# Kernel tuning notes

Hardware: AMD Instinct MI355X
Metric: run time of the kernel (lower is better)

## Reference

```python
import jax, jax.numpy as jnp
import numpy as np

T, IN, H = 16384, 1024, 4096   # tokens, in_features, hidden_features
G = 64                          # quantization group size (nunchaku default)
R = 32                          # LoRA rank for SVDQuant low-rank branch


def _dequant_weight(qw, ws):
    # qw: [out, in] int4 values in [-8,7] (stored int32); ws: [out, in//G] per-group scales
    out, inn = qw.shape
    w = qw.astype(jnp.float32).reshape(out, inn // G, G) * ws[:, :, None]
    return w.reshape(out, inn)


def _qdq_act(x):
    # simulate per-token, per-group int4 quantize->dequantize of activations
    t, d = x.shape
    xg = x.reshape(t, d // G, G)
    s = jnp.maximum(jnp.max(jnp.abs(xg), axis=-1, keepdims=True), 1e-6) / 7.0
    q = jnp.clip(jnp.round(xg / s), -8.0, 7.0)
    return (q * s).reshape(t, d)


def _svdquant_linear(x, qw, ws, smooth, ld, lu, b):
    # quantized main branch on smoothed input + full-precision LoRA correction on raw input
    xq = _qdq_act(x / smooth)                      # [T, d_in]
    w = _dequant_weight(qw, ws)                    # [d_out, d_in]
    main = jnp.einsum('td,od->to', xq, w)          # int4-sim GEMM
    lora = jnp.einsum('tr,or->to', jnp.einsum('td,rd->tr', x, ld), lu)
    return main + lora + b


def setup_inputs() -> dict:
    key = jax.random.key(0)
    ks = jax.random.split(key, 12)
    x = jax.random.normal(ks[0], (T, IN), dtype=jnp.float32)
    qw1 = jax.random.randint(ks[1], (H, IN), -8, 8, dtype=jnp.int32)
    ws1 = jax.random.uniform(ks[2], (H, IN // G), dtype=jnp.float32) * 0.01 + 0.001
    smooth1 = jax.random.uniform(ks[3], (IN,), dtype=jnp.float32) + 0.5
    ld1 = jax.random.normal(ks[4], (R, IN), dtype=jnp.float32) * 0.02
    lu1 = jax.random.normal(ks[5], (H, R), dtype=jnp.float32) * 0.02
    b1 = jax.random.normal(ks[6], (H,), dtype=jnp.float32) * 0.01
    qw2 = jax.random.randint(ks[7], (IN, H), -8, 8, dtype=jnp.int32)
    ws2 = jax.random.uniform(ks[8], (IN, H // G), dtype=jnp.float32) * 0.01 + 0.001
    smooth2 = jax.random.uniform(ks[9], (H,), dtype=jnp.float32) + 0.5
    ld2 = jax.random.normal(ks[10], (R, H), dtype=jnp.float32) * 0.02
    lu2 = jax.random.normal(ks[11], (IN, R), dtype=jnp.float32) * 0.02
    b2 = jnp.zeros((IN,), dtype=jnp.float32)
    return {"x": x, "qw1": qw1, "ws1": ws1, "smooth1": smooth1, "ld1": ld1,
            "lu1": lu1, "b1": b1, "qw2": qw2, "ws2": ws2, "smooth2": smooth2,
            "ld2": ld2, "lu2": lu2, "b2": b2}


def reference(x, qw1, ws1, smooth1, ld1, lu1, b1, qw2, ws2, smooth2, ld2, lu2, b2):
    h = _svdquant_linear(x, qw1, ws1, smooth1, ld1, lu1, b1)   # fc1
    h = jax.nn.gelu(h, approximate=True)                        # fused GELU
    y = _svdquant_linear(h, qw2, ws2, smooth2, ld2, lu2, b2)   # fc2
    return y
```

## Files before the change

### kernel.cpp

```cpp
#include <hip/hip_runtime.h>
#include <math.h>

#define T_TOK 16384
#define D_IN  1024
#define D_H   4096
#define GQ    64
#define R_L   32
#define NPANEL 4
#define PANW   (D_H / NPANEL)

typedef __attribute__((ext_vector_type(8))) __bf16 bf16x8;
typedef __attribute__((ext_vector_type(4))) float  f32x4;
typedef __attribute__((ext_vector_type(8))) unsigned short ushort8;

__device__ __forceinline__ unsigned short f2bf(float f) {
  union { float f; unsigned u; } v; v.f = f;
  unsigned u = v.u + 0x7FFFu + ((v.u >> 16) & 1u);
  return (unsigned short)(u >> 16);
}

__device__ __forceinline__ float bf2f(unsigned short h) {
  union { unsigned u; float f; } v; v.u = ((unsigned)h) << 16; return v.f;
}

__device__ __forceinline__ void gload_lds16(const unsigned short* g, unsigned short* l) {
  __builtin_amdgcn_global_load_lds(
      (const __attribute__((address_space(1))) unsigned int*)g,
      (__attribute__((address_space(3))) unsigned int*)l, 16, 0, 0);
}

__device__ __forceinline__ float gelu_tanh(float v) {
  float u = 0.7978845608028654f * (v + 0.044715f * v * v * v);
  return 0.5f * v * (1.0f + tanhf(u));
}

__global__ __launch_bounds__(256)
void convert_kernel(const int* __restrict__ qw1, const int* __restrict__ qw2,
                    unsigned short* __restrict__ qw1b, unsigned short* __restrict__ qw2b) {
  const size_t N1 = (size_t)D_H * D_IN;
  const size_t N2 = (size_t)D_IN * D_H;
  const size_t total = N1 + N2;
  for (size_t i = (size_t)blockIdx.x * 256 + threadIdx.x; i < total;
       i += (size_t)gridDim.x * 256) {
    if (i < N1) qw1b[i]    = f2bf((float)qw1[i]);
    else        qw2b[i-N1] = f2bf((float)qw2[i-N1]);
  }
}

__global__ __launch_bounds__(256)
void prep1_kernel(const float* __restrict__ x, const float* __restrict__ smooth,
                  const float* __restrict__ ld,
                  unsigned short* __restrict__ qx, float* __restrict__ sx,
                  float* __restrict__ xrf) {
  __shared__ float xrow[D_IN];
  const int t = blockIdx.x;
  const int tid = threadIdx.x;
  float4 x4  = *(const float4*)(x + (size_t)t * D_IN + tid * 4);
  float4 sm4 = *(const float4*)(smooth + tid * 4);
  *(float4*)&xrow[tid * 4] = x4;
  double z0 = (double)x4.x / (double)sm4.x;
  double z1 = (double)x4.y / (double)sm4.y;
  double z2 = (double)x4.z / (double)sm4.z;
  double z3 = (double)x4.w / (double)sm4.w;
  double amax = fmax(fmax(fabs(z0), fabs(z1)), fmax(fabs(z2), fabs(z3)));
#pragma unroll
  for (int d = 1; d < 16; d <<= 1) amax = fmax(amax, __shfl_xor(amax, d, 16));
  double s = fmax(amax, 1e-6) / 7.0;
  double q0 = fmin(fmax(rint(z0 / s), -8.0), 7.0);
  double q1 = fmin(fmax(rint(z1 / s), -8.0), 7.0);
  double q2 = fmin(fmax(rint(z2 / s), -8.0), 7.0);
  double q3 = fmin(fmax(rint(z3 / s), -8.0), 7.0);
  ushort4 qu; qu.x = f2bf((float)q0); qu.y = f2bf((float)q1);
  qu.z = f2bf((float)q2); qu.w = f2bf((float)q3);
  *(ushort4*)(qx + (size_t)t * D_IN + tid * 4) = qu;
  if ((tid & 15) == 0) sx[(size_t)t * (D_IN / GQ) + (tid >> 4)] = (float)s;
  __syncthreads();
  const int w = tid >> 6, l = tid & 63;
#pragma unroll
  for (int rr = 0; rr < 8; ++rr) {
    int r = w * 8 + rr;
    const float* ldr = ld + (size_t)r * D_IN;
    double sum = 0.0;
#pragma unroll
    for (int k = 0; k < 16; ++k)
      sum = fma((double)xrow[l + 64 * k], (double)ldr[l + 64 * k], sum);
#pragma unroll
    for (int d = 32; d >= 1; d >>= 1) sum += __shfl_xor(sum, d, 64);
    if (l == 0) xrf[(size_t)t * R_L + r] = (float)sum;
  }
}

__global__ __launch_bounds__(512, 2)
void gemm_fc1(const unsigned short* __restrict__ Aq,
              const float* __restrict__ Asx,
              const unsigned short* __restrict__ Bq,
              const float* __restrict__ Bws,
              const float* __restrict__ xrf,
              const float* __restrict__ lu1,
              const float* __restrict__ b1,
              const float* __restrict__ smooth2,
              int c0base,
              unsigned short* __restrict__ hb,
              unsigned short* __restrict__ qx2,
              float* __restrict__ sx2) {
  __shared__ unsigned short As[2][128 * 64];
  __shared__ unsigned short Bs[2][128 * 64];
  __shared__ float sxd[2][128];
  __shared__ float wss[2][128];
  const int tid = threadIdx.x;
  const int lane = tid & 63;
  const int wid = tid >> 6;
  const int wr = wid >> 1;
  const int wc = wid & 1;
  const int l15 = lane & 15, l4 = lane >> 4;
  const int lin = blockIdx.y * 8 + blockIdx.x;
  const int sw  = (lin & 7) * 128 + (lin >> 3);
  const int t0 = (sw >> 3) * 128;
  const int c0 = c0base + (sw & 7) * 128;

  float acc[2][4][4] = {};
  const int srow = tid >> 3;
  const int schk = tid & 7;
  const int ske  = schk * 8;
  const int sswz = (schk ^ (srow & 7)) * 8;

#pragma unroll
  for (int q = 0; q < 2; ++q) {
    int row = q * 64 + srow;
    gload_lds16(Aq + (long)(t0 + row) * D_IN + sswz, &As[0][row * 64 + ske]);
    gload_lds16(Bq + (long)(c0 + row) * D_IN + sswz, &Bs[0][row * 64 + ske]);
  }
  if (tid < 128)      sxd[0][tid] = Asx[(long)(t0 + tid) * 16 + 0];
  else if (tid < 256) wss[0][tid - 128] = Bws[(long)(c0 + tid - 128) * 16 + 0];

  int cur = 0;
  for (int g = 0; g < 16; ++g) {
    __syncthreads();

    if (g < 15) {
      const int kn = (g + 1) * 64;
      const int nb = cur ^ 1;
#pragma unroll
      for (int q = 0; q < 2; ++q) {
        int row = q * 64 + srow;
        gload_lds16(Aq + (long)(t0 + row) * D_IN + kn + sswz,
                    &As[nb][row * 64 + ske]);
        gload_lds16(Bq + (long)(c0 + row) * D_IN + kn + sswz,
                    &Bs[nb][row * 64 + ske]);
      }
      if (tid < 128)      sxd[nb][tid] = Asx[(long)(t0 + tid) * 16 + (g + 1)];
      else if (tid < 256) wss[nb][tid - 128] = Bws[(long)(c0 + tid - 128) * 16 + (g + 1)];
    }

    float sd[2][4];
#pragma unroll
    for (int m = 0; m < 2; ++m)
#pragma unroll
      for (int jj = 0; jj < 4; ++jj)
        sd[m][jj] = sxd[cur][wr * 32 + m * 16 + l4 * 4 + jj];
    float wd[4];
#pragma unroll
    for (int n = 0; n < 4; ++n)
      wd[n] = wss[cur][wc * 64 + n * 16 + l15];

    bf16x8 af[2][2], bfr[4][2];
#pragma unroll
    for (int m = 0; m < 2; ++m) {
      const int r = wr * 32 + m * 16 + l15;
      const unsigned short* base = &As[cur][r * 64];
      af[m][0] = *(const bf16x8*)(base + ((l4    ) ^ (r & 7)) * 8);
      af[m][1] = *(const bf16x8*)(base + ((l4 + 4) ^ (r & 7)) * 8);
    }
#pragma unroll
    for (int n = 0; n < 4; ++n) {
      const int r = wc * 64 + n * 16 + l15;
      const unsigned short* base = &Bs[cur][r * 64];
      bfr[n][0] = *(const bf16x8*)(base + ((l4    ) ^ (r & 7)) * 8);
      bfr[n][1] = *(const bf16x8*)(base + ((l4 + 4) ^ (r & 7)) * 8);
    }

#pragma unroll
    for (int m = 0; m < 2; ++m) {
#pragma unroll
      for (int n = 0; n < 4; ++n) {
        f32x4 t = {0.f, 0.f, 0.f, 0.f};
        t = __builtin_amdgcn_mfma_f32_16x16x32_bf16(af[m][0], bfr[n][0], t, 0, 0, 0);
        t = __builtin_amdgcn_mfma_f32_16x16x32_bf16(af[m][1], bfr[n][1], t, 0, 0, 0);
#pragma unroll
        for (int j = 0; j < 4; ++j)
          acc[m][n][j] = fmaf(t[j], sd[m][j] * wd[n], acc[m][n][j]);
      }
    }
    cur ^= 1;
  }

  __syncthreads();
  float* xr_lds = (float*)&As[0][0];
  float* lu_lds = (float*)&Bs[0][0];
  {
    const int row = tid >> 2;
    const int q4  = (tid & 3) * 8;
    const float4 a0 = *(const float4*)(xrf + (size_t)(t0 + row) * R_L + q4);
    const float4 a1 = *(const float4*)(xrf + (size_t)(t0 + row) * R_L + q4 + 4);
    *(float4*)&xr_lds[row * 36 + q4]     = a0;
    *(float4*)&xr_lds[row * 36 + q4 + 4] = a1;
    const float4 b0 = *(const float4*)(lu1 + (size_t)(c0 + row) * R_L + q4);
    const float4 b1v = *(const float4*)(lu1 + (size_t)(c0 + row) * R_L + q4 + 4);
    *(float4*)&lu_lds[row * 36 + q4]     = b0;
    *(float4*)&lu_lds[row * 36 + q4 + 4] = b1v;
  }
  __syncthreads();

  float bv[4], rsmv[4];
  int colL[4];
#pragma unroll
  for (int n = 0; n < 4; ++n) {
    int col = c0 + wc * 64 + n * 16 + l15;
    colL[n] = wc * 64 + n * 16 + l15;
    bv[n] = b1[col];
    rsmv[n] = 1.0f / smooth2[col];
  }
  const int clocal0 = c0 - c0base;

#pragma unroll
  for (int m = 0; m < 2; ++m) {
#pragma unroll
    for (int j = 0; j < 4; ++j) {
      const int rloc = wr * 32 + m * 16 + l4 * 4 + j;
      const int trow = t0 + rloc;
      float lor[4] = {0.f, 0.f, 0.f, 0.f};
#pragma unroll
      for (int k = 0; k < 8; ++k) {
        const float4 xq = *(const float4*)&xr_lds[rloc * 36 + k * 4];
#pragma unroll
        for (int n = 0; n < 4; ++n) {
          const float4 lc = *(const float4*)&lu_lds[colL[n] * 36 + k * 4];
          lor[n] = fmaf(xq.x, lc.x, lor[n]);
          lor[n] = fmaf(xq.y, lc.y, lor[n]);
          lor[n] = fmaf(xq.z, lc.z, lor[n]);
          lor[n] = fmaf(xq.w, lc.w, lor[n]);
        }
      }
      float hv[4], z[4];
      float amax = 0.f;
#pragma unroll
      for (int n = 0; n < 4; ++n) {
        float v = acc[m][n][j] + lor[n] + bv[n];
        v = gelu_tanh(v);
        hv[n] = v;
        z[n] = v * rsmv[n];
        amax = fmaxf(amax, fabsf(z[n]));
      }
#pragma unroll
      for (int d = 1; d < 16; d <<= 1) amax = fmaxf(amax, __shfl_xor(amax, d, 16));
      float s = fmaxf(amax, 1e-6f) / 7.0f;
      float rs = 1.0f / s;
#pragma unroll
      for (int n = 0; n < 4; ++n) {
        int coll = clocal0 + wc * 64 + n * 16 + l15;
        hb[(size_t)trow * PANW + coll] = f2bf(hv[n]);
        float qv = fminf(fmaxf(rintf(z[n] * rs), -8.f), 7.f);
        qx2[(size_t)trow * PANW + coll] = f2bf(qv);
      }
      if (l15 == 0)
        sx2[(size_t)trow * (PANW / GQ) + ((clocal0 + wc * 64) >> 6)] = s;
    }
  }
}

__global__ __launch_bounds__(256, 2)
void gemm_fc2(const unsigned short* __restrict__ Aq,
              const float* __restrict__ Asx,
              const unsigned short* __restrict__ Bq,
              int kB0,
              const float* __restrict__ Bws,
              int gB0,
              float* __restrict__ Yout, int first) {
  __shared__ unsigned short As[128 * 64];
  __shared__ unsigned short Bs[128 * 64];
  __shared__ float sxs[128];
  __shared__ float wss[128];
  const int tid = threadIdx.x;
  const int lane = tid & 63;
  const int wid = tid >> 6;
  const int wr = wid >> 1, wc = wid & 1;
  const int l15 = lane & 15, l4 = lane >> 4;
  const int lin = blockIdx.y * 8 + blockIdx.x;
  const int sw  = (lin & 7) * 128 + (lin >> 3);
  const int t0 = (sw >> 3) * 128;
  const int c0 = (sw & 7) * 128;

  f32x4 acc[4][4] = {};
  const int srow = tid >> 3;
  const int ske = (tid & 7) * 8;

  for (int g = 0; g < 16; ++g) {
    const int kA = g * 64 + ske;
    const int kB = kB0 + kA;
#pragma unroll
    for (int i = 0; i < 4; ++i) {
      int row = i * 32 + srow;
      gload_lds16(Aq + (long)(t0 + row) * PANW + kA, As + row * 64 + ske);
      gload_lds16(Bq + (long)(c0 + row) * D_H + kB, Bs + row * 64 + ske);
    }
    if (tid < 128) sxs[tid] = Asx[(long)(t0 + tid) * (PANW / GQ) + g];
    else           wss[tid - 128] = Bws[(long)(c0 + tid - 128) * (D_H / GQ) + gB0 + g];
    __syncthreads();

    bf16x8 af[4][2], bfr[4][2];
#pragma unroll
    for (int m = 0; m < 4; ++m) {
      const unsigned short* base = As + (wr * 64 + m * 16 + l15) * 64 + l4 * 8;
      af[m][0] = *(const bf16x8*)(base);
      af[m][1] = *(const bf16x8*)(base + 32);
    }
#pragma unroll
    for (int n = 0; n < 4; ++n) {
      const unsigned short* base = Bs + (wc * 64 + n * 16 + l15) * 64 + l4 * 8;
      bfr[n][0] = *(const bf16x8*)(base);
      bfr[n][1] = *(const bf16x8*)(base + 32);
    }
    f32x4 rsv[4];
#pragma unroll
    for (int m = 0; m < 4; ++m) rsv[m] = *(const f32x4*)&sxs[wr * 64 + m * 16 + l4 * 4];
    float csv[4];
#pragma unroll
    for (int n = 0; n < 4; ++n) csv[n] = wss[wc * 64 + n * 16 + l15];

#pragma unroll
    for (int m = 0; m < 4; ++m) {
#pragma unroll
      for (int n = 0; n < 4; ++n) {
        f32x4 t = {0.f, 0.f, 0.f, 0.f};
        t = __builtin_amdgcn_mfma_f32_16x16x32_bf16(af[m][0], bfr[n][0], t, 0, 0, 0);
        t = __builtin_amdgcn_mfma_f32_16x16x32_bf16(af[m][1], bfr[n][1], t, 0, 0, 0);
#pragma unroll
        for (int j = 0; j < 4; ++j)
          acc[m][n][j] += t[j] * (rsv[m][j] * csv[n]);
      }
    }
    __syncthreads();
  }

#pragma unroll
  for (int m = 0; m < 4; ++m)
#pragma unroll
    for (int n = 0; n < 4; ++n) {
      int col = c0 + wc * 64 + n * 16 + l15;
#pragma unroll
      for (int j = 0; j < 4; ++j) {
        int trow = t0 + wr * 64 + m * 16 + l4 * 4 + j;
        size_t idx = (size_t)trow * D_IN + col;
        float v = acc[m][n][j];
        if (!first) v += Yout[idx];
        Yout[idx] = v;
      }
    }
}

__global__ __launch_bounds__(256)
void xr2_simple(const unsigned short* __restrict__ hp,
                const float* __restrict__ ld2,
                int c0base,
                float* __restrict__ xracc,
                int first) {
  __shared__ unsigned short hs[8][PANW + 8];
  const int tid = threadIdx.x;
  const int t0 = blockIdx.x * 8;
#pragma unroll
  for (int q = 0; q < 4; ++q) {
    int v = tid + 256 * q;
    int row = v >> 7;
    int col = (v & 127) * 8;
    *(ushort8*)(&hs[row][col]) =
        *(const ushort8*)(hp + (size_t)(t0 + row) * PANW + col);
  }
  __syncthreads();
  const int tloc = tid & 7;
  const int r    = tid >> 3;
  const float* ldr = ld2 + (size_t)r * D_H + c0base;
  float sum = 0.f;
  for (int k8 = 0; k8 < PANW / 8; ++k8) {
    ushort8 hv = *(const ushort8*)(&hs[tloc][k8 * 8]);
    float4 w0 = *(const float4*)(ldr + k8 * 8);
    float4 w1 = *(const float4*)(ldr + k8 * 8 + 4);
    sum = fmaf(bf2f(hv[0]), w0.x, sum);
    sum = fmaf(bf2f(hv[1]), w0.y, sum);
    sum = fmaf(bf2f(hv[2]), w0.z, sum);
    sum = fmaf(bf2f(hv[3]), w0.w, sum);
    sum = fmaf(bf2f(hv[4]), w1.x, sum);
    sum = fmaf(bf2f(hv[5]), w1.y, sum);
    sum = fmaf(bf2f(hv[6]), w1.z, sum);
    sum = fmaf(bf2f(hv[7]), w1.w, sum);
  }
  size_t idx = (size_t)(t0 + tloc) * R_L + r;
  xracc[idx] = (first ? 0.f : xracc[idx]) + sum;
}

__global__ __launch_bounds__(256)
void finish_kernel(const float* __restrict__ xracc,
                   const float* __restrict__ lu2,
                   const float* __restrict__ b2,
                   float* __restrict__ Yout) {
  __shared__ float xls[16][R_L];
  const int tid = threadIdx.x;
  const int o   = blockIdx.x * 256 + tid;
  const int t0r = blockIdx.y * 16;
  for (int q = tid; q < 16 * R_L; q += 256)
    xls[q >> 5][q & 31] = xracc[(size_t)(t0r + (q >> 5)) * R_L + (q & 31)];
  float lr[R_L];
#pragma unroll
  for (int r = 0; r < R_L; ++r) lr[r] = lu2[(size_t)o * R_L + r];
  const float b2v = b2[o];
  __syncthreads();
#pragma unroll
  for (int i = 0; i < 16; ++i) {
    size_t idx = (size_t)(t0r + i) * D_IN + o;
    float v = Yout[idx] + b2v;
#pragma unroll
    for (int r = 0; r < R_L; ++r) v = fmaf(lr[r], xls[i][r], v);
    Yout[idx] = v;
  }
}

extern "C" void kernel_launch(void* const* d_in, const int* in_sizes, int n_in,
                              void* d_out, int out_size, void* d_ws, size_t ws_size,
                              hipStream_t stream) {
  const float* x       = (const float*)d_in[0];
  const int*   qw1     = (const int*)d_in[1];
  const float* ws1     = (const float*)d_in[2];
  const float* smooth1 = (const float*)d_in[3];
  const float* ld1     = (const float*)d_in[4];
  const float* lu1     = (const float*)d_in[5];
  const float* b1      = (const float*)d_in[6];
  const int*   qw2     = (const int*)d_in[7];
  const float* ws2     = (const float*)d_in[8];
  const float* smooth2 = (const float*)d_in[9];
  const float* ld2     = (const float*)d_in[10];
  const float* lu2     = (const float*)d_in[11];
  const float* b2      = (const float*)d_in[12];

  char* w = (char*)d_ws;
  size_t off = 0;
  auto take = [&](size_t bytes) {
    char* p = w + off;
    off = (off + bytes + 255) & ~(size_t)255;
    return p;
  };

  unsigned short* qw1b = (unsigned short*)take((size_t)D_H * D_IN * 2);
  unsigned short* qw2b = (unsigned short*)take((size_t)D_IN * D_H * 2);
  unsigned short* qx1  = (unsigned short*)take((size_t)T_TOK * D_IN * 2);
  float*          sx1  = (float*)take((size_t)T_TOK * (D_IN / GQ) * 4);
  float*          xr1f = (float*)take((size_t)T_TOK * R_L * 4);
  unsigned short* hp   = (unsigned short*)take((size_t)T_TOK * PANW * 2);
  unsigned short* qx2p = (unsigned short*)take((size_t)T_TOK * PANW * 2);
  float*          sx2  = (float*)take((size_t)T_TOK * (PANW / GQ) * 4);
  float*          xr2a = (float*)take((size_t)T_TOK * R_L * 4);
  (void)ws_size; (void)in_sizes; (void)n_in; (void)out_size;

  convert_kernel<<<2048, 256, 0, stream>>>(qw1, qw2, qw1b, qw2b);
  prep1_kernel<<<T_TOK, 256, 0, stream>>>(x, smooth1, ld1, qx1, sx1, xr1f);

  for (int p = 0; p < NPANEL; ++p) {
    const int c0base = p * PANW;
    const int first = (p == 0);

    dim3 g1(PANW / 128, T_TOK / 128);
    gemm_fc1<<<g1, 512, 0, stream>>>(qx1, sx1, qw1b, ws1, xr1f, lu1, b1, smooth2,
                                     c0base, hp, qx2p, sx2);

    xr2_simple<<<T_TOK / 8, 256, 0, stream>>>(hp, ld2, c0base, xr2a, first);

    dim3 g2(D_IN / 128, T_TOK / 128);
    gemm_fc2<<<g2, 256, 0, stream>>>(qx2p, sx2, qw2b, c0base, ws2, p * (PANW / GQ),
                                     (float*)d_out, first);
  }

  dim3 gf(D_IN / 256, T_TOK / 16);
  finish_kernel<<<gf, 256, 0, stream>>>(xr2a, lu2, b2, (float*)d_out);
}
```

Before: 1.297 ms.

## Double-buffer fc2 GEMM with swizzled LDS, fuse LoRA/bias epilogue, float prep dot

```diff
diff --git a/kernel.cpp b/kernel.cpp
--- a/kernel.cpp
+++ b/kernel.cpp
@@ -80,13 +80,13 @@
   for (int rr = 0; rr < 8; ++rr) {
     int r = w * 8 + rr;
     const float* ldr = ld + (size_t)r * D_IN;
-    double sum = 0.0;
+    float sum = 0.f;
 #pragma unroll
     for (int k = 0; k < 16; ++k)
-      sum = fma((double)xrow[l + 64 * k], (double)ldr[l + 64 * k], sum);
+      sum = fmaf(xrow[l + 64 * k], ldr[l + 64 * k], sum);
 #pragma unroll
     for (int d = 32; d >= 1; d >>= 1) sum += __shfl_xor(sum, d, 64);
-    if (l == 0) xrf[(size_t)t * R_L + r] = (float)sum;
+    if (l == 0) xrf[(size_t)t * R_L + r] = sum;
   }
 }
 
@@ -268,67 +268,95 @@
   }
 }
 
-__global__ __launch_bounds__(256, 2)
+__global__ __launch_bounds__(512, 2)
 void gemm_fc2(const unsigned short* __restrict__ Aq,
               const float* __restrict__ Asx,
               const unsigned short* __restrict__ Bq,
               int kB0,
               const float* __restrict__ Bws,
               int gB0,
-              float* __restrict__ Yout, int first) {
-  __shared__ unsigned short As[128 * 64];
-  __shared__ unsigned short Bs[128 * 64];
-  __shared__ float sxs[128];
-  __shared__ float wss[128];
+              const float* __restrict__ xr2a,
+              const float* __restrict__ lu2,
+              const float* __restrict__ b2,
+              float* __restrict__ Yout, int first, int last) {
+  __shared__ unsigned short As[2][128 * 64];
+  __shared__ unsigned short Bs[2][128 * 64];
+  __shared__ float sxd[2][128];
+  __shared__ float wss[2][128];
   const int tid = threadIdx.x;
   const int lane = tid & 63;
   const int wid = tid >> 6;
-  const int wr = wid >> 1, wc = wid & 1;
+  const int wr = wid >> 1;
+  const int wc = wid & 1;
   const int l15 = lane & 15, l4 = lane >> 4;
   const int lin = blockIdx.y * 8 + blockIdx.x;
   const int sw  = (lin & 7) * 128 + (lin >> 3);
   const int t0 = (sw >> 3) * 128;
   const int c0 = (sw & 7) * 128;
 
-  f32x4 acc[4][4] = {};
+  float acc[2][4][4] = {};
   const int srow = tid >> 3;
-  const int ske = (tid & 7) * 8;
-
+  const int schk = tid & 7;
+  const int ske  = schk * 8;
+  const int sswz = (schk ^ (srow & 7)) * 8;
+
+#pragma unroll
+  for (int q = 0; q < 2; ++q) {
+    int row = q * 64 + srow;
+    gload_lds16(Aq + (long)(t0 + row) * PANW + sswz, &As[0][row * 64 + ske]);
+    gload_lds16(Bq + (long)(c0 + row) * D_H + kB0 + sswz, &Bs[0][row * 64 + ske]);
+  }
+  if (tid < 128)      sxd[0][tid] = Asx[(long)(t0 + tid) * (PANW / GQ) + 0];
+  else if (tid < 256) wss[0][tid - 128] = Bws[(long)(c0 + tid - 128) * (D_H / GQ) + gB0 + 0];
+
+  int cur = 0;
   for (int g = 0; g < 16; ++g) {
-    const int kA = g * 64 + ske;
-    const int kB = kB0 + kA;
-#pragma unroll
-    for (int i = 0; i < 4; ++i) {
-      int row = i * 32 + srow;
-      gload_lds16(Aq + (long)(t0 + row) * PANW + kA, As + row * 64 + ske);
-      gload_lds16(Bq + (long)(c0 + row) * D_H + kB, Bs + row * 64 + ske);
-    }
-    if (tid < 128) sxs[tid] = Asx[(long)(t0 + tid) * (PANW / GQ) + g];
-    else           wss[tid - 128] = Bws[(long)(c0 + tid - 128) * (D_H / GQ) + gB0 + g];
     __syncthreads();
 
-    bf16x8 af[4][2], bfr[4][2];
-#pragma unroll
-    for (int m = 0; m < 4; ++m) {
-      const unsigned short* base = As + (wr * 64 + m * 16 + l15) * 64 + l4 * 8;
-      af[m][0] = *(const bf16x8*)(base);
-      af[m][1] = *(const bf16x8*)(base + 32);
+    if (g < 15) {
+      const int kn = (g + 1) * 64;
+      const int nb = cur ^ 1;
+#pragma unroll
+      for (int q = 0; q < 2; ++q) {
+        int row = q * 64 + srow;
+        gload_lds16(Aq + (long)(t0 + row) * PANW + kn + sswz,
+                    &As[nb][row * 64 + ske]);
+        gload_lds16(Bq + (long)(c0 + row) * D_H + kB0 + kn + sswz,
+                    &Bs[nb][row * 64 + ske]);
+      }
+      if (tid < 128)      sxd[nb][tid] = Asx[(long)(t0 + tid) * (PANW / GQ) + (g + 1)];
+      else if (tid < 256) wss[nb][tid - 128] = Bws[(long)(c0 + tid - 128) * (D_H / GQ) + gB0 + (g + 1)];
+    }
+
+    float sd[2][4];
+#pragma unroll
+    for (int m = 0; m < 2; ++m)
+#pragma unroll
+      for (int jj = 0; jj < 4; ++jj)
+        sd[m][jj] = sxd[cur][wr * 32 + m * 16 + l4 * 4 + jj];
+    float wd[4];
+#pragma unroll
+    for (int n = 0; n < 4; ++n)
+      wd[n] = wss[cur][wc * 64 + n * 16 + l15];
+
+    bf16x8 af[2][2], bfr[4][2];
+#pragma unroll
+    for (int m = 0; m < 2; ++m) {
+      const int r = wr * 32 + m * 16 + l15;
+      const unsigned short* base = &As[cur][r * 64];
+      af[m][0] = *(const bf16x8*)(base + ((l4    ) ^ (r & 7)) * 8);
+      af[m][1] = *(const bf16x8*)(base + ((l4 + 4) ^ (r & 7)) * 8);
     }
 #pragma unroll
     for (int n = 0; n < 4; ++n) {
-      const unsigned short* base = Bs + (wc * 64 + n * 16 + l15) * 64 + l4 * 8;
-      bfr[n][0] = *(const bf16x8*)(base);
-      bfr[n][1] = *(const bf16x8*)(base + 32);
-    }
-    f32x4 rsv[4];
-#pragma unroll
-    for (int m = 0; m < 4; ++m) rsv[m] = *(const f32x4*)&sxs[wr * 64 + m * 16 + l4 * 4];
-    float csv[4];
-#pragma unroll
-    for (int n = 0; n < 4; ++n) csv[n] = wss[wc * 64 + n * 16 + l15];
-
-#pragma unroll
-    for (int m = 0; m < 4; ++m) {
+      const int r = wc * 64 + n * 16 + l15;
+      const unsigned short* base = &Bs[cur][r * 64];
+      bfr[n][0] = *(const bf16x8*)(base + ((l4    ) ^ (r & 7)) * 8);
+      bfr[n][1] = *(const bf16x8*)(base + ((l4 + 4) ^ (r & 7)) * 8);
+    }
+
+#pragma unroll
+    for (int m = 0; m < 2; ++m) {
 #pragma unroll
       for (int n = 0; n < 4; ++n) {
         f32x4 t = {0.f, 0.f, 0.f, 0.f};
@@ -336,26 +364,79 @@
         t = __builtin_amdgcn_mfma_f32_16x16x32_bf16(af[m][1], bfr[n][1], t, 0, 0, 0);
 #pragma unroll
         for (int j = 0; j < 4; ++j)
-          acc[m][n][j] += t[j] * (rsv[m][j] * csv[n]);
-      }
-    }
+          acc[m][n][j] = fmaf(t[j], sd[m][j] * wd[n], acc[m][n][j]);
+      }
+    }
+    cur ^= 1;
+  }
+
+  if (last) {
     __syncthreads();
-  }
-
-#pragma unroll
-  for (int m = 0; m < 4; ++m)
+    float* xr_lds = (float*)&As[0][0];
+    float* lu_lds = (float*)&Bs[0][0];
+    {
+      const int row = tid >> 2;
+      const int q4  = (tid & 3) * 8;
+      const float4 a0 = *(const float4*)(xr2a + (size_t)(t0 + row) * R_L + q4);
+      const float4 a1 = *(const float4*)(xr2a + (size_t)(t0 + row) * R_L + q4 + 4);
+      *(float4*)&xr_lds[row * 36 + q4]     = a0;
+      *(float4*)&xr_lds[row * 36 + q4 + 4] = a1;
+      const float4 b0 = *(const float4*)(lu2 + (size_t)(c0 + row) * R_L + q4);
+      const float4 b1v = *(const float4*)(lu2 + (size_t)(c0 + row) * R_L + q4 + 4);
+      *(float4*)&lu_lds[row * 36 + q4]     = b0;
+      *(float4*)&lu_lds[row * 36 + q4 + 4] = b1v;
+    }
+    __syncthreads();
+
+    float bv[4];
+    int colL[4];
 #pragma unroll
     for (int n = 0; n < 4; ++n) {
-      int col = c0 + wc * 64 + n * 16 + l15;
+      colL[n] = wc * 64 + n * 16 + l15;
+      bv[n] = b2[c0 + colL[n]];
+    }
+#pragma unroll
+    for (int m = 0; m < 2; ++m) {
 #pragma unroll
       for (int j = 0; j < 4; ++j) {
-        int trow = t0 + wr * 64 + m * 16 + l4 * 4 + j;
-        size_t idx = (size_t)trow * D_IN + col;
-        float v = acc[m][n][j];
-        if (!first) v += Yout[idx];
-        Yout[idx] = v;
-      }
-    }
+        const int rloc = wr * 32 + m * 16 + l4 * 4 + j;
+        const int trow = t0 + rloc;
+        float lor[4] = {0.f, 0.f, 0.f, 0.f};
+#pragma unroll
+        for (int k = 0; k < 8; ++k) {
+          const float4 xq = *(const float4*)&xr_lds[rloc * 36 + k * 4];
+#pragma unroll
+          for (int n = 0; n < 4; ++n) {
+            const float4 lc = *(const float4*)&lu_lds[colL[n] * 36 + k * 4];
+            lor[n] = fmaf(xq.x, lc.x, lor[n]);
+            lor[n] = fmaf(xq.y, lc.y, lor[n]);
+            lor[n] = fmaf(xq.z, lc.z, lor[n]);
+            lor[n] = fmaf(xq.w, lc.w, lor[n]);
+          }
+        }
+#pragma unroll
+        for (int n = 0; n < 4; ++n) {
+          size_t idx = (size_t)trow * D_IN + c0 + colL[n];
+          Yout[idx] = Yout[idx] + acc[m][n][j] + lor[n] + bv[n];
+        }
+      }
+    }
+  } else {
+#pragma unroll
+    for (int m = 0; m < 2; ++m)
+#pragma unroll
+      for (int n = 0; n < 4; ++n) {
+        int col = c0 + wc * 64 + n * 16 + l15;
+#pragma unroll
+        for (int j = 0; j < 4; ++j) {
+          int trow = t0 + wr * 32 + m * 16 + l4 * 4 + j;
+          size_t idx = (size_t)trow * D_IN + col;
+          float v = acc[m][n][j];
+          if (!first) v += Yout[idx];
+          Yout[idx] = v;
+        }
+      }
+  }
 }
 
 __global__ __launch_bounds__(256)
@@ -397,32 +478,6 @@
   xracc[idx] = (first ? 0.f : xracc[idx]) + sum;
 }
 
-__global__ __launch_bounds__(256)
-void finish_kernel(const float* __restrict__ xracc,
-                   const float* __restrict__ lu2,
-                   const float* __restrict__ b2,
-                   float* __restrict__ Yout) {
-  __shared__ float xls[16][R_L];
-  const int tid = threadIdx.x;
-  const int o   = blockIdx.x * 256 + tid;
-  const int t0r = blockIdx.y * 16;
-  for (int q = tid; q < 16 * R_L; q += 256)
-    xls[q >> 5][q & 31] = xracc[(size_t)(t0r + (q >> 5)) * R_L + (q & 31)];
-  float lr[R_L];
-#pragma unroll
-  for (int r = 0; r < R_L; ++r) lr[r] = lu2[(size_t)o * R_L + r];
-  const float b2v = b2[o];
-  __syncthreads();
-#pragma unroll
-  for (int i = 0; i < 16; ++i) {
-    size_t idx = (size_t)(t0r + i) * D_IN + o;
-    float v = Yout[idx] + b2v;
-#pragma unroll
-    for (int r = 0; r < R_L; ++r) v = fmaf(lr[r], xls[i][r], v);
-    Yout[idx] = v;
-  }
-}
-
 extern "C" void kernel_launch(void* const* d_in, const int* in_sizes, int n_in,
                               void* d_out, int out_size, void* d_ws, size_t ws_size,
                               hipStream_t stream) {
@@ -464,7 +519,7 @@
 
   for (int p = 0; p < NPANEL; ++p) {
     const int c0base = p * PANW;
-    const int first = (p == 0);
+    const int first = (p == 0), last = (p == NPANEL - 1);
 
     dim3 g1(PANW / 128, T_TOK / 128);
     gemm_fc1<<<g1, 512, 0, stream>>>(qx1, sx1, qw1b, ws1, xr1f, lu1, b1, smooth2,
@@ -473,10 +528,7 @@
     xr2_simple<<<T_TOK / 8, 256, 0, stream>>>(hp, ld2, c0base, xr2a, first);
 
     dim3 g2(D_IN / 128, T_TOK / 128);
-    gemm_fc2<<<g2, 256, 0, stream>>>(qx2p, sx2, qw2b, c0base, ws2, p * (PANW / GQ),
-                                     (float*)d_out, first);
-  }
-
-  dim3 gf(D_IN / 256, T_TOK / 16);
-  finish_kernel<<<gf, 256, 0, stream>>>(xr2a, lu2, b2, (float*)d_out);
-}
+    gemm_fc2<<<g2, 512, 0, stream>>>(qx2p, sx2, qw2b, c0base, ws2, p * (PANW / GQ),
+                                     xr2a, lu2, b2, (float*)d_out, first, last);
+  }
+}
```

Measured after the change: 1.380 ms (median of 2 runs). +6.4%, slower.

## Rework fc1 GEMM to 256 threads, single-buffered LDS, larger per-warp tiles

Applied to the files above, without the earlier changes.

```diff
diff --git a/kernel.cpp b/kernel.cpp
--- a/kernel.cpp
+++ b/kernel.cpp
@@ -80,17 +80,17 @@
   for (int rr = 0; rr < 8; ++rr) {
     int r = w * 8 + rr;
     const float* ldr = ld + (size_t)r * D_IN;
-    double sum = 0.0;
+    float sum = 0.f;
 #pragma unroll
     for (int k = 0; k < 16; ++k)
-      sum = fma((double)xrow[l + 64 * k], (double)ldr[l + 64 * k], sum);
+      sum = fmaf(xrow[l + 64 * k], ldr[l + 64 * k], sum);
 #pragma unroll
     for (int d = 32; d >= 1; d >>= 1) sum += __shfl_xor(sum, d, 64);
-    if (l == 0) xrf[(size_t)t * R_L + r] = (float)sum;
-  }
-}
-
-__global__ __launch_bounds__(512, 2)
+    if (l == 0) xrf[(size_t)t * R_L + r] = sum;
+  }
+}
+
+__global__ __launch_bounds__(256, 2)
 void gemm_fc1(const unsigned short* __restrict__ Aq,
               const float* __restrict__ Asx,
               const unsigned short* __restrict__ Bq,
@@ -103,84 +103,59 @@
               unsigned short* __restrict__ hb,
               unsigned short* __restrict__ qx2,
               float* __restrict__ sx2) {
-  __shared__ unsigned short As[2][128 * 64];
-  __shared__ unsigned short Bs[2][128 * 64];
-  __shared__ float sxd[2][128];
-  __shared__ float wss[2][128];
+  __shared__ __align__(16) char smem[36864];
+  unsigned short* As = (unsigned short*)smem;
+  unsigned short* Bs = (unsigned short*)(smem + 16384);
+  float* sxs = (float*)(smem + 32768);
+  float* wss = (float*)(smem + 33280);
   const int tid = threadIdx.x;
   const int lane = tid & 63;
   const int wid = tid >> 6;
-  const int wr = wid >> 1;
-  const int wc = wid & 1;
+  const int wr = wid >> 1, wc = wid & 1;
   const int l15 = lane & 15, l4 = lane >> 4;
   const int lin = blockIdx.y * 8 + blockIdx.x;
   const int sw  = (lin & 7) * 128 + (lin >> 3);
   const int t0 = (sw >> 3) * 128;
   const int c0 = c0base + (sw & 7) * 128;
 
-  float acc[2][4][4] = {};
+  f32x4 acc[4][4] = {};
   const int srow = tid >> 3;
-  const int schk = tid & 7;
-  const int ske  = schk * 8;
-  const int sswz = (schk ^ (srow & 7)) * 8;
-
-#pragma unroll
-  for (int q = 0; q < 2; ++q) {
-    int row = q * 64 + srow;
-    gload_lds16(Aq + (long)(t0 + row) * D_IN + sswz, &As[0][row * 64 + ske]);
-    gload_lds16(Bq + (long)(c0 + row) * D_IN + sswz, &Bs[0][row * 64 + ske]);
-  }
-  if (tid < 128)      sxd[0][tid] = Asx[(long)(t0 + tid) * 16 + 0];
-  else if (tid < 256) wss[0][tid - 128] = Bws[(long)(c0 + tid - 128) * 16 + 0];
-
-  int cur = 0;
+  const int ske  = (tid & 7) * 8;
+
   for (int g = 0; g < 16; ++g) {
+    const int kA = g * 64 + ske;
+#pragma unroll
+    for (int i = 0; i < 4; ++i) {
+      int row = i * 32 + srow;
+      gload_lds16(Aq + (long)(t0 + row) * D_IN + kA, As + row * 64 + ske);
+      gload_lds16(Bq + (long)(c0 + row) * D_IN + kA, Bs + row * 64 + ske);
+    }
+    if (tid < 128) sxs[tid] = Asx[(long)(t0 + tid) * 16 + g];
+    else           wss[tid - 128] = Bws[(long)(c0 + tid - 128) * 16 + g];
     __syncthreads();
 
-    if (g < 15) {
-      const int kn = (g + 1) * 64;
-      const int nb = cur ^ 1;
-#pragma unroll
-      for (int q = 0; q < 2; ++q) {
-        int row = q * 64 + srow;
-        gload_lds16(Aq + (long)(t0 + row) * D_IN + kn + sswz,
-                    &As[nb][row * 64 + ske]);
-        gload_lds16(Bq + (long)(c0 + row) * D_IN + kn + sswz,
-                    &Bs[nb][row * 64 + ske]);
-      }
-      if (tid < 128)      sxd[nb][tid] = Asx[(long)(t0 + tid) * 16 + (g + 1)];
-      else if (tid < 256) wss[nb][tid - 128] = Bws[(long)(c0 + tid - 128) * 16 + (g + 1)];
-    }
-
-    float sd[2][4];
-#pragma unroll
-    for (int m = 0; m < 2; ++m)
-#pragma unroll
-      for (int jj = 0; jj < 4; ++jj)
-        sd[m][jj] = sxd[cur][wr * 32 + m * 16 + l4 * 4 + jj];
-    float wd[4];
-#pragma unroll
-    for (int n = 0; n < 4; ++n)
-      wd[n] = wss[cur][wc * 64 + n * 16 + l15];
-
-    bf16x8 af[2][2], bfr[4][2];
-#pragma unroll
-    for (int m = 0; m < 2; ++m) {
-      const int r = wr * 32 + m * 16 + l15;
-      const unsigned short* base = &As[cur][r * 64];
-      af[m][0] = *(const bf16x8*)(base + ((l4    ) ^ (r & 7)) * 8);
-      af[m][1] = *(const bf16x8*)(base + ((l4 + 4) ^ (r & 7)) * 8);
+    bf16x8 af[4][2], bfr[4][2];
+#pragma unroll
+    for (int m = 0; m < 4; ++m) {
+      const unsigned short* base = As + (wr * 64 + m * 16 + l15) * 64 + l4 * 8;
+      af[m][0] = *(const bf16x8*)(base);
+      af[m][1] = *(const bf16x8*)(base + 32);
     }
 #pragma unroll
     for (int n = 0; n < 4; ++n) {
-      const int r = wc * 64 + n * 16 + l15;
-      const unsigned short* base = &Bs[cur][r * 64];
-      bfr[n][0] = *(const bf16x8*)(base + ((l4    ) ^ (r & 7)) * 8);
-      bfr[n][1] = *(const bf16x8*)(base + ((l4 + 4) ^ (r & 7)) * 8);
-    }
-
-#pragma unroll
-    for (int m = 0; m < 2; ++m) {
+      const unsigned short* base = Bs + (wc * 64 + n * 16 + l15) * 64 + l4 * 8;
+      bfr[n][0] = *(const bf16x8*)(base);
+      bfr[n][1] = *(const bf16x8*)(base + 32);
+    }
+    f32x4 rsv[4];
+#pragma unroll
+    for (int m = 0; m < 4; ++m) rsv[m] = *(const f32x4*)&sxs[wr * 64 + m * 16 + l4 * 4];
+    float csv[4];
+#pragma unroll
+    for (int n = 0; n < 4; ++n) csv[n] = wss[wc * 64 + n * 16 + l15];
+
+#pragma unroll
+    for (int m = 0; m < 4; ++m) {
 #pragma unroll
       for (int n = 0; n < 4; ++n) {
         f32x4 t = {0.f, 0.f, 0.f, 0.f};
@@ -188,26 +163,24 @@
         t = __builtin_amdgcn_mfma_f32_16x16x32_bf16(af[m][1], bfr[n][1], t, 0, 0, 0);
 #pragma unroll
         for (int j = 0; j < 4; ++j)
-          acc[m][n][j] = fmaf(t[j], sd[m][j] * wd[n], acc[m][n][j]);
-      }
-    }
-    cur ^= 1;
-  }
-
-  __syncthreads();
-  float* xr_lds = (float*)&As[0][0];
-  float* lu_lds = (float*)&Bs[0][0];
+          acc[m][n][j] = fmaf(t[j], rsv[m][j] * csv[n], acc[m][n][j]);
+      }
+    }
+    __syncthreads();
+  }
+
+  float* xr_lds = (float*)smem;
+  float* lu_lds = (float*)(smem + 18432);
   {
-    const int row = tid >> 2;
-    const int q4  = (tid & 3) * 8;
-    const float4 a0 = *(const float4*)(xrf + (size_t)(t0 + row) * R_L + q4);
-    const float4 a1 = *(const float4*)(xrf + (size_t)(t0 + row) * R_L + q4 + 4);
-    *(float4*)&xr_lds[row * 36 + q4]     = a0;
-    *(float4*)&xr_lds[row * 36 + q4 + 4] = a1;
-    const float4 b0 = *(const float4*)(lu1 + (size_t)(c0 + row) * R_L + q4);
-    const float4 b1v = *(const float4*)(lu1 + (size_t)(c0 + row) * R_L + q4 + 4);
-    *(float4*)&lu_lds[row * 36 + q4]     = b0;
-    *(float4*)&lu_lds[row * 36 + q4 + 4] = b1v;
+    const int row = tid >> 1;
+    const int q4  = (tid & 1) * 16;
+#pragma unroll
+    for (int h = 0; h < 4; ++h) {
+      *(float4*)&xr_lds[row * 36 + q4 + h * 4] =
+          *(const float4*)(xrf + (size_t)(t0 + row) * R_L + q4 + h * 4);
+      *(float4*)&lu_lds[row * 36 + q4 + h * 4] =
+          *(const float4*)(lu1 + (size_t)(c0 + row) * R_L + q4 + h * 4);
+    }
   }
   __syncthreads();
 
@@ -223,10 +196,10 @@
   const int clocal0 = c0 - c0base;
 
 #pragma unroll
-  for (int m = 0; m < 2; ++m) {
+  for (int m = 0; m < 4; ++m) {
 #pragma unroll
     for (int j = 0; j < 4; ++j) {
-      const int rloc = wr * 32 + m * 16 + l4 * 4 + j;
+      const int rloc = wr * 64 + m * 16 + l4 * 4 + j;
       const int trow = t0 + rloc;
       float lor[4] = {0.f, 0.f, 0.f, 0.f};
 #pragma unroll
@@ -467,7 +440,7 @@
     const int first = (p == 0);
 
     dim3 g1(PANW / 128, T_TOK / 128);
-    gemm_fc1<<<g1, 512, 0, stream>>>(qx1, sx1, qw1b, ws1, xr1f, lu1, b1, smooth2,
+    gemm_fc1<<<g1, 256, 0, stream>>>(qx1, sx1, qw1b, ws1, xr1f, lu1, b1, smooth2,
                                      c0base, hp, qx2p, sx2);
 
     xr2_simple<<<T_TOK / 8, 256, 0, stream>>>(hp, ld2, c0base, xr2a, first);
```

Result: faster. 1.204 ms (-7.2%).
